# Performance work log

Measured on AMD Instinct MI355X. Metric: run time of the kernel, lower is better.

## Reference

```python
import jax, jax.numpy as jnp
import numpy as np

N, H, C, K = 8192, 1024, 1024, 32  # tokens, nhid, ncls, words-per-class (vocab = C*K = 32768)
R = 0.1  # init_weights uniform range


def setup_inputs() -> dict:
    key = jax.random.key(0)
    k0, k1, k2, k3 = jax.random.split(key, 4)
    x = jax.random.normal(k0, (N, H), jnp.float32)
    cls = jax.random.randint(k1, (N,), 0, C)  # per-token class id (derived from word2cls[target])
    W_cls = jax.random.uniform(k2, (C, H), jnp.float32, -R, R)
    b_cls = jnp.zeros((C,), jnp.float32)
    W_words = jax.random.uniform(k3, (C, K, H), jnp.float32, -R, R)  # stacked per-class Linear weights
    b_words = jnp.zeros((C, K), jnp.float32)
    return {"x": x, "cls": cls, "W_cls": W_cls, "b_cls": b_cls,
            "W_words": W_words, "b_words": b_words}


def reference(x, cls, W_cls, b_cls, W_words, b_words):
    # Class head: nn.Linear(nhid, ncls) over all tokens -> [N, C]
    p_class = x @ W_cls.T + b_cls
    # Per-class word heads: original gathers tokens per class (index_select) and
    # applies that class's nn.Linear(nhid, K). Equivalent grouped form: gather each
    # token's class weights and do a batched matvec. p_words[i] are the within-class
    # logits of token i under class cls[i] (same math, token order instead of
    # dict-of-classes order).
    Wg = W_words[cls]                                   # [N, K, H]
    p_words = jnp.einsum('nh,nkh->nk', x, Wg) + b_words[cls]  # [N, K]
    return p_class, p_words
```

## Files before the change

kernel.cpp:

```cpp
#include <hip/hip_runtime.h>
#include <stdint.h>

#define HDIM 1024
#define CDIM 1024
#define KW   32
#define CAP  64

typedef unsigned short u16;
typedef __attribute__((ext_vector_type(8))) short bf16x8;
typedef __attribute__((ext_vector_type(4))) float f32x4;

#define GLDS16(gp, lp)                                                                    \
  __builtin_amdgcn_global_load_lds((const __attribute__((address_space(1))) void*)(gp),   \
                                   (__attribute__((address_space(3))) void*)(lp), 16, 0, 0)

__device__ __forceinline__ u16 f2bf(float f) {
  union { float f; unsigned u; } v; v.f = f;
  unsigned r = v.u + 0x7FFFu + ((v.u >> 16) & 1u);
  return (u16)(r >> 16);
}

__device__ __forceinline__ bf16x8 pack8(float4 a, float4 b) {
  bf16x8 r;
  r[0] = (short)f2bf(a.x); r[1] = (short)f2bf(a.y);
  r[2] = (short)f2bf(a.z); r[3] = (short)f2bf(a.w);
  r[4] = (short)f2bf(b.x); r[5] = (short)f2bf(b.y);
  r[6] = (short)f2bf(b.z); r[7] = (short)f2bf(b.w);
  return r;
}

__global__ __launch_bounds__(256) void convert_and_zero(const float* __restrict__ x,
                                                        u16* __restrict__ xbf, int n4x,
                                                        const float* __restrict__ Wc,
                                                        u16* __restrict__ wbf, int n4w,
                                                        int* __restrict__ cursor) {
  const int tid0 = blockIdx.x * 256 + threadIdx.x;
  if (tid0 < CDIM) cursor[tid0] = 0;
  const int total = n4x + n4w;
  const int stride = gridDim.x * 256;
  for (int j = tid0; j < total; j += stride) {
    float4 v;
    if (j < n4x) v = ((const float4*)x)[j];
    else         v = ((const float4*)Wc)[j - n4x];
    ushort4 o;
    o.x = f2bf(v.x); o.y = f2bf(v.y); o.z = f2bf(v.z); o.w = f2bf(v.w);
    if (j < n4x) ((ushort4*)xbf)[j] = o;
    else         ((ushort4*)wbf)[j - n4x] = o;
  }
}

__global__ __launch_bounds__(256) void scatter_kernel(const int* __restrict__ cls, int N,
                                                      int* __restrict__ cursor,
                                                      int* __restrict__ toklist) {
  const int i = blockIdx.x * 256 + threadIdx.x;
  if (i < N) {
    const int c = cls[i];
    const int pos = atomicAdd(&cursor[c], 1);
    if (pos < CAP) toklist[c * CAP + pos] = i;
  }
}

#define GEMM_STAGE(BUF, KT)                                       \
  GLDS16(xb + ga0 + (KT), As[BUF] + (size_t)c0 * 8);              \
  GLDS16(xb + ga1 + (KT), As[BUF] + (size_t)c1 * 8);              \
  GLDS16(wb + gb0 + (KT), Bs[BUF] + (size_t)c0 * 8);              \
  GLDS16(wb + gb1 + (KT), Bs[BUF] + (size_t)c1 * 8);

#define GEMM_COMPUTE(BUF)                                                                  \
  {                                                                                        \
    bf16x8 a[4], b[4];                                                                     \
    _Pragma("unroll") for (int m = 0; m < 4; m++)                                          \
      a[m] = *(const bf16x8*)&As[BUF][(wr * 64 + m * 16 + fr) * 32 + koff];                \
    _Pragma("unroll") for (int n = 0; n < 4; n++)                                          \
      b[n] = *(const bf16x8*)&Bs[BUF][(wc * 64 + n * 16 + fr) * 32 + koff];                \
    _Pragma("unroll") for (int m = 0; m < 4; m++)                                          \
      _Pragma("unroll") for (int n = 0; n < 4; n++)                                        \
        acc[m][n] = __builtin_amdgcn_mfma_f32_16x16x32_bf16(a[m], b[n], acc[m][n], 0, 0, 0); \
  }

__global__ __launch_bounds__(256) void gemm_bf16_kernel(const u16* __restrict__ xb,
                                                        const u16* __restrict__ wb,
                                                        const float* __restrict__ bcls,
                                                        float* __restrict__ out) {
  __shared__ u16 As[2][128 * 32];
  __shared__ u16 Bs[2][128 * 32];
  const int tid  = threadIdx.x;
  const int lane = tid & 63;
  const int wid  = tid >> 6;
  const int wr   = wid >> 1, wc = wid & 1;
  const int bm = blockIdx.x, bn = blockIdx.y;

  const int c0 = tid, c1 = tid + 256;
  const size_t ga0 = (size_t)(bm * 128 + (c0 >> 2)) * HDIM + (c0 & 3) * 8;
  const size_t ga1 = (size_t)(bm * 128 + (c1 >> 2)) * HDIM + (c1 & 3) * 8;
  const size_t gb0 = (size_t)(bn * 128 + (c0 >> 2)) * HDIM + (c0 & 3) * 8;
  const size_t gb1 = (size_t)(bn * 128 + (c1 >> 2)) * HDIM + (c1 & 3) * 8;

  f32x4 acc[4][4] = {};

  const int fr   = lane & 15;
  const int koff = (lane >> 4) * 8;

  GEMM_STAGE(0, 0);
  __syncthreads();
  int cur = 0;
#pragma unroll 2
  for (int kt = 0; kt < HDIM - 32; kt += 32) {
    GEMM_STAGE(cur ^ 1, kt + 32);
    GEMM_COMPUTE(cur);
    __syncthreads();
    cur ^= 1;
  }
  GEMM_COMPUTE(cur);

  const int crow = (lane >> 4) * 4;
  const int ccol = lane & 15;
#pragma unroll
  for (int n = 0; n < 4; n++) {
    const int col   = bn * 128 + wc * 64 + n * 16 + ccol;
    const float bias = bcls[col];
#pragma unroll
    for (int m = 0; m < 4; m++) {
      const int row0 = bm * 128 + wr * 64 + m * 16 + crow;
#pragma unroll
      for (int r = 0; r < 4; r++)
        out[(size_t)(row0 + r) * CDIM + col] = acc[m][n][r] + bias;
    }
  }
}

__global__ __launch_bounds__(256) void words_mfma(const u16* __restrict__ xbf,
                                                  const float* __restrict__ Ww,
                                                  const float* __restrict__ bw,
                                                  const int* __restrict__ toklist,
                                                  const int* __restrict__ cursor,
                                                  float* __restrict__ outw) {
  const int c = blockIdx.x;
  const int count = min(cursor[c], CAP);
  if (count <= 0) return;
  __shared__ float red[4][2][16][16];
  __shared__ int toks[16];
  const int tid  = threadIdx.x;
  const int lane = tid & 63, wave = tid >> 6;
  const int fr   = lane & 15;
  const int koff = (lane >> 4) * 8;
  const float* Wc = Ww + (size_t)c * KW * HDIM;
  const int k0 = wave * 256;

  for (int base = 0; base < count; base += 16) {
    const int nt = min(16, count - base);
    __syncthreads();
    if (tid < 16) toks[tid] = toklist[c * CAP + base + min(tid, nt - 1)];
    __syncthreads();
    const u16* arow = xbf + (size_t)toks[fr] * HDIM;
    const float* b0row = Wc + (size_t)fr * HDIM;
    const float* b1row = Wc + (size_t)(16 + fr) * HDIM;
    f32x4 acc0 = {}, acc1 = {};
#pragma unroll
    for (int ks = 0; ks < 8; ks++) {
      const int kt = k0 + ks * 32 + koff;
      bf16x8 a = *(const bf16x8*)(arow + kt);
      float4 b0a = *(const float4*)(b0row + kt);
      float4 b0b = *(const float4*)(b0row + kt + 4);
      float4 b1a = *(const float4*)(b1row + kt);
      float4 b1b = *(const float4*)(b1row + kt + 4);
      bf16x8 b0 = pack8(b0a, b0b);
      bf16x8 b1 = pack8(b1a, b1b);
      acc0 = __builtin_amdgcn_mfma_f32_16x16x32_bf16(a, b0, acc0, 0, 0, 0);
      acc1 = __builtin_amdgcn_mfma_f32_16x16x32_bf16(a, b1, acc1, 0, 0, 0);
    }
    const int rb = (lane >> 4) * 4, cc = lane & 15;
#pragma unroll
    for (int r = 0; r < 4; r++) {
      red[wave][0][rb + r][cc] = acc0[r];
      red[wave][1][rb + r][cc] = acc1[r];
    }
    __syncthreads();
    const int row = tid >> 4, col = tid & 15;
#pragma unroll
    for (int wcx = 0; wcx < 2; wcx++) {
      float s = 0.f;
#pragma unroll
      for (int w = 0; w < 4; w++) s += red[w][wcx][row][col];
      if (row < nt) {
        const int word = wcx * 16 + col;
        outw[(size_t)toks[row] * KW + word] = s + bw[c * KW + word];
      }
    }
  }
}

__global__ __launch_bounds__(256) void words_kernel(const float* __restrict__ x,
                                                    const int* __restrict__ cls,
                                                    const float* __restrict__ Ww,
                                                    const float* __restrict__ bw,
                                                    float* __restrict__ outw) {
  const int n    = blockIdx.x;
  const int c    = cls[n];
  const int lane = threadIdx.x & 63;
  const int wave = threadIdx.x >> 6;
  const float4* xr = (const float4*)(x + (size_t)n * HDIM);
  float4 xv[4];
#pragma unroll
  for (int i = 0; i < 4; i++) xv[i] = xr[lane + 64 * i];
  const float* Wc = Ww + (size_t)c * KW * HDIM;
#pragma unroll
  for (int wi = 0; wi < 8; wi++) {
    const int w = wave * 8 + wi;
    const float4* wrp = (const float4*)(Wc + (size_t)w * HDIM);
    float s = 0.f;
#pragma unroll
    for (int i = 0; i < 4; i++) {
      float4 wv = wrp[lane + 64 * i];
      s += xv[i].x * wv.x + xv[i].y * wv.y + xv[i].z * wv.z + xv[i].w * wv.w;
    }
#pragma unroll
    for (int off = 32; off > 0; off >>= 1) s += __shfl_down(s, off);
    if (lane == 0) outw[(size_t)n * KW + w] = s + bw[c * KW + w];
  }
}

__global__ __launch_bounds__(256) void gemm_f32_naive(const float* __restrict__ x,
                                                      const float* __restrict__ Wc,
                                                      const float* __restrict__ bc,
                                                      float* __restrict__ out) {
  __shared__ float xs[HDIM];
  const int n = blockIdx.x;
  const int tid = threadIdx.x;
  ((float4*)xs)[tid] = ((const float4*)(x + (size_t)n * HDIM))[tid];
  __syncthreads();
  for (int c = tid; c < CDIM; c += 256) {
    const float* wr = Wc + (size_t)c * HDIM;
    float s = 0.f;
    for (int h = 0; h < HDIM; h += 4) {
      float4 wv = *(const float4*)(wr + h);
      s += xs[h] * wv.x + xs[h + 1] * wv.y + xs[h + 2] * wv.z + xs[h + 3] * wv.w;
    }
    out[(size_t)n * CDIM + c] = s + bc[c];
  }
}

extern "C" void kernel_launch(void* const* d_in, const int* in_sizes, int n_in,
                              void* d_out, int out_size, void* d_ws, size_t ws_size,
                              hipStream_t stream) {
  const float* x   = (const float*)d_in[0];
  const int*   cls = (const int*)d_in[1];
  const float* Wc  = (const float*)d_in[2];
  const float* bc  = (const float*)d_in[3];
  const float* Ww  = (const float*)d_in[4];
  const float* bw  = (const float*)d_in[5];
  float* out = (float*)d_out;
  const int N = in_sizes[0] / HDIM;
  float* outw = out + (size_t)N * CDIM;

  const size_t bf_bytes  = ((size_t)N * HDIM + (size_t)CDIM * HDIM) * sizeof(u16);
  const size_t ints_off  = (bf_bytes + 63) & ~(size_t)63;
  const size_t need_all  = ints_off + ((size_t)CDIM + (size_t)CDIM * CAP) * sizeof(int);

  if (ws_size >= need_all && (N % 128) == 0) {
    u16* xbf = (u16*)d_ws;
    u16* wbf = xbf + (size_t)N * HDIM;
    int* cursor  = (int*)((char*)d_ws + ints_off);
    int* toklist = cursor + CDIM;

    convert_and_zero<<<2048, 256, 0, stream>>>(x, xbf, N * HDIM / 4,
                                               Wc, wbf, CDIM * HDIM / 4, cursor);
    scatter_kernel<<<(N + 255) / 256, 256, 0, stream>>>(cls, N, cursor, toklist);
    dim3 grid(N / 128, CDIM / 128);
    gemm_bf16_kernel<<<grid, 256, 0, stream>>>(xbf, wbf, bc, out);
    words_mfma<<<CDIM, 256, 0, stream>>>(xbf, Ww, bw, toklist, cursor, outw);
  } else {
    gemm_f32_naive<<<N, 256, 0, stream>>>(x, Wc, bc, out);
    words_kernel<<<N, 256, 0, stream>>>(x, cls, Ww, bw, outw);
  }
}
```

Baseline: 66.71 us.

## Merge class GEMM and word-head kernels into one interleaved launch

Combines the bf16 class-head GEMM and the per-class word-head MFMA kernel into a single kernel whose blocks are split by block index. When the GEMM block count is half the class count, one of every three blocks does a GEMM tile and the other two do word heads, so compute-bound and memory-bound work run on the GPU at the same time. This removes one kernel launch and the tail gap between the two kernels. In exchange, every block reserves the larger GEMM shared-memory footprint, which can lower occupancy for the word-head blocks.

Measured after the change: 72.05 us. +8.0%, slower.

```diff
diff --git a/kernel.cpp b/kernel.cpp
--- a/kernel.cpp
+++ b/kernel.cpp
@@ -61,34 +61,35 @@
 }
 
 #define GEMM_STAGE(BUF, KT)                                       \
-  GLDS16(xb + ga0 + (KT), As[BUF] + (size_t)c0 * 8);              \
-  GLDS16(xb + ga1 + (KT), As[BUF] + (size_t)c1 * 8);              \
-  GLDS16(wb + gb0 + (KT), Bs[BUF] + (size_t)c0 * 8);              \
-  GLDS16(wb + gb1 + (KT), Bs[BUF] + (size_t)c1 * 8);
-
-#define GEMM_COMPUTE(BUF)                                                                  \
-  {                                                                                        \
-    bf16x8 a[4], b[4];                                                                     \
-    _Pragma("unroll") for (int m = 0; m < 4; m++)                                          \
-      a[m] = *(const bf16x8*)&As[BUF][(wr * 64 + m * 16 + fr) * 32 + koff];                \
-    _Pragma("unroll") for (int n = 0; n < 4; n++)                                          \
-      b[n] = *(const bf16x8*)&Bs[BUF][(wc * 64 + n * 16 + fr) * 32 + koff];                \
-    _Pragma("unroll") for (int m = 0; m < 4; m++)                                          \
-      _Pragma("unroll") for (int n = 0; n < 4; n++)                                        \
+  GLDS16(xb + ga0 + (KT), As + (BUF) * 4096 + (size_t)c0 * 8);    \
+  GLDS16(xb + ga1 + (KT), As + (BUF) * 4096 + (size_t)c1 * 8);    \
+  GLDS16(wb + gb0 + (KT), Bs + (BUF) * 4096 + (size_t)c0 * 8);    \
+  GLDS16(wb + gb1 + (KT), Bs + (BUF) * 4096 + (size_t)c1 * 8);
+
+#define GEMM_COMPUTE(BUF)                                                                    \
+  {                                                                                          \
+    bf16x8 a[4], b[4];                                                                       \
+    _Pragma("unroll") for (int m = 0; m < 4; m++)                                            \
+      a[m] = *(const bf16x8*)&As[(BUF) * 4096 + (wr * 64 + m * 16 + fr) * 32 + koff];        \
+    _Pragma("unroll") for (int n = 0; n < 4; n++)                                            \
+      b[n] = *(const bf16x8*)&Bs[(BUF) * 4096 + (wc * 64 + n * 16 + fr) * 32 + koff];        \
+    _Pragma("unroll") for (int m = 0; m < 4; m++)                                            \
+      _Pragma("unroll") for (int n = 0; n < 4; n++)                                          \
         acc[m][n] = __builtin_amdgcn_mfma_f32_16x16x32_bf16(a[m], b[n], acc[m][n], 0, 0, 0); \
   }
 
-__global__ __launch_bounds__(256) void gemm_bf16_kernel(const u16* __restrict__ xb,
-                                                        const u16* __restrict__ wb,
-                                                        const float* __restrict__ bcls,
-                                                        float* __restrict__ out) {
-  __shared__ u16 As[2][128 * 32];
-  __shared__ u16 Bs[2][128 * 32];
+__device__ __forceinline__ void gemm_block(int gid, char* smem,
+                                           const u16* __restrict__ xb,
+                                           const u16* __restrict__ wb,
+                                           const float* __restrict__ bcls,
+                                           float* __restrict__ out) {
+  u16* As = (u16*)smem;
+  u16* Bs = (u16*)smem + 8192;
   const int tid  = threadIdx.x;
   const int lane = tid & 63;
   const int wid  = tid >> 6;
   const int wr   = wid >> 1, wc = wid & 1;
-  const int bm = blockIdx.x, bn = blockIdx.y;
+  const int bm = gid >> 3, bn = gid & 7;
 
   const int c0 = tid, c1 = tid + 256;
   const size_t ga0 = (size_t)(bm * 128 + (c0 >> 2)) * HDIM + (c0 & 3) * 8;
@@ -129,17 +130,17 @@
   }
 }
 
-__global__ __launch_bounds__(256) void words_mfma(const u16* __restrict__ xbf,
-                                                  const float* __restrict__ Ww,
-                                                  const float* __restrict__ bw,
-                                                  const int* __restrict__ toklist,
-                                                  const int* __restrict__ cursor,
-                                                  float* __restrict__ outw) {
-  const int c = blockIdx.x;
+__device__ __forceinline__ void words_block(int c, char* smem,
+                                            const u16* __restrict__ xbf,
+                                            const float* __restrict__ Ww,
+                                            const float* __restrict__ bw,
+                                            const int* __restrict__ toklist,
+                                            const int* __restrict__ cursor,
+                                            float* __restrict__ outw) {
   const int count = min(cursor[c], CAP);
   if (count <= 0) return;
-  __shared__ float red[4][2][16][16];
-  __shared__ int toks[16];
+  float* red = (float*)smem;
+  int* toks  = (int*)(smem + 8192);
   const int tid  = threadIdx.x;
   const int lane = tid & 63, wave = tid >> 6;
   const int fr   = lane & 15;
@@ -172,8 +173,8 @@
     const int rb = (lane >> 4) * 4, cc = lane & 15;
 #pragma unroll
     for (int r = 0; r < 4; r++) {
-      red[wave][0][rb + r][cc] = acc0[r];
-      red[wave][1][rb + r][cc] = acc1[r];
+      red[((wave * 2 + 0) * 16 + rb + r) * 16 + cc] = acc0[r];
+      red[((wave * 2 + 1) * 16 + rb + r) * 16 + cc] = acc1[r];
     }
     __syncthreads();
     const int row = tid >> 4, col = tid & 15;
@@ -181,12 +182,32 @@
     for (int wcx = 0; wcx < 2; wcx++) {
       float s = 0.f;
 #pragma unroll
-      for (int w = 0; w < 4; w++) s += red[w][wcx][row][col];
+      for (int w = 0; w < 4; w++) s += red[((w * 2 + wcx) * 16 + row) * 16 + col];
       if (row < nt) {
         const int word = wcx * 16 + col;
         outw[(size_t)toks[row] * KW + word] = s + bw[c * KW + word];
       }
     }
+  }
+}
+
+__global__ __launch_bounds__(256) void mega_kernel(const u16* __restrict__ xbf,
+                                                   const u16* __restrict__ wbf,
+                                                   const float* __restrict__ bc,
+                                                   float* __restrict__ out,
+                                                   const float* __restrict__ Ww,
+                                                   const float* __restrict__ bw,
+                                                   const int* __restrict__ toklist,
+                                                   const int* __restrict__ cursor,
+                                                   float* __restrict__ outw, int nbg) {
+  __shared__ __align__(16) char smem[32832];
+  const int bid = blockIdx.x;
+  if (2 * nbg == CDIM) {
+    if (bid % 3 == 0) gemm_block(bid / 3, smem, xbf, wbf, bc, out);
+    else              words_block(bid - bid / 3 - 1, smem, xbf, Ww, bw, toklist, cursor, outw);
+  } else {
+    if (bid < nbg) gemm_block(bid, smem, xbf, wbf, bc, out);
+    else           words_block(bid - nbg, smem, xbf, Ww, bw, toklist, cursor, outw);
   }
 }
 
@@ -266,9 +287,9 @@
     convert_and_zero<<<2048, 256, 0, stream>>>(x, xbf, N * HDIM / 4,
                                                Wc, wbf, CDIM * HDIM / 4, cursor);
     scatter_kernel<<<(N + 255) / 256, 256, 0, stream>>>(cls, N, cursor, toklist);
-    dim3 grid(N / 128, CDIM / 128);
-    gemm_bf16_kernel<<<grid, 256, 0, stream>>>(xbf, wbf, bc, out);
-    words_mfma<<<CDIM, 256, 0, stream>>>(xbf, Ww, bw, toklist, cursor, outw);
+    const int nbg = (N / 128) * (CDIM / 128);
+    mega_kernel<<<nbg + CDIM, 256, 0, stream>>>(xbf, wbf, bc, out, Ww, bw,
+                                                toklist, cursor, outw, nbg);
   } else {
     gemm_f32_naive<<<N, 256, 0, stream>>>(x, Wc, bc, out);
     words_kernel<<<N, 256, 0, stream>>>(x, cls, Ww, bw, outw);
```
